# Performance work log

Measured on AMD Instinct MI355X. Metric: run time of the kernel, lower is better.

## Reference

```python
import jax, jax.numpy as jnp
import numpy as np

B, S, E = 4, 2048, 512
H, D = 8, 64
MIN_W, MAX_W = 256, 1024
EPS = 1e-6


def setup_inputs() -> dict:
    key = jax.random.key(0)
    ks = jax.random.split(key, 9)
    w = lambda k, shp: jax.random.normal(k, shp, dtype=jnp.float32) * 0.02
    return {
        "x": jax.random.normal(ks[0], (B, S, E), dtype=jnp.float32),
        "rms1_w": jnp.ones((E,), jnp.float32),
        "rms2_w": jnp.ones((E,), jnp.float32),
        "qkv_w": w(ks[1], (3 * E, E)),
        "out_w": w(ks[2], (E, E)),
        "cs_w1": w(ks[3], (E // 4, E)),
        "cs_w2": w(ks[4], (1, E // 4)),
        "gate_w": w(ks[5], (2304, E)),
        "up_w": w(ks[6], (2304, E)),
        "down_w": w(ks[7], (E, 2304)),
    }


def _rmsnorm(x, w):
    rms = jax.lax.rsqrt(jnp.mean(x * x, axis=-1, keepdims=True) + EPS)
    return x * rms * w


def _rotate_half(x):
    x1 = x[..., ::2]
    x2 = x[..., 1::2]
    return jnp.stack((-x2, x1), axis=-1).reshape(x.shape)


def reference(x, rms1_w, rms2_w, qkv_w, out_w, cs_w1, cs_w2, gate_w, up_w, down_w):
    # --- pre-norm ---
    h = _rmsnorm(x, rms1_w)                                  # [B,S,E]
    # --- qkv ---
    qkv = h @ qkv_w.T                                        # [B,S,3E]
    qkv = qkv.reshape(B, S, 3, H, D).transpose(2, 0, 3, 1, 4)
    q, k, v = qkv[0], qkv[1], qkv[2]                         # [B,H,S,D]
    # --- RoPE (cat-freqs cos/sin + interleaved rotate_half, as in source) ---
    inv_freq = 1.0 / (10000.0 ** (jnp.arange(0, D, 2, dtype=jnp.float32) / D))
    pos = jnp.arange(S, dtype=jnp.float32)
    freqs = jnp.outer(pos, inv_freq)                         # [S,D/2]
    emb = jnp.concatenate([freqs, freqs], axis=-1)           # [S,D]
    cos = jnp.cos(emb)[None, None]
    sin = jnp.sin(emb)[None, None]
    q = q * cos + _rotate_half(q) * sin
    k = k * cos + _rotate_half(k) * sin
    # --- attention scores ---
    scale = D ** -0.5
    scores = jnp.einsum("bhqd,bhkd->bhqk", q, k) * scale     # [B,H,S,S]
    # --- complexity -> dynamic window size ---
    n = S * E
    mu = jnp.mean(h, axis=(1, 2), keepdims=True)
    var = jnp.sum((h - mu) ** 2, axis=(1, 2)) / (n - 1)      # unbiased, per batch
    var_norm = jax.nn.sigmoid(var * 10.0 - 5.0)
    xm = jnp.mean(h, axis=1)                                 # [B,E]
    learned = jax.nn.sigmoid((jax.nn.silu(xm @ cs_w1.T)) @ cs_w2.T)[:, 0]
    complexity = (var_norm + learned) / 2.0                  # [B]
    ws_f = MIN_W + jnp.mean(complexity) * (MAX_W - MIN_W)
    ws = ws_f.astype(jnp.int32)                              # trunc, like .int()
    ws = jnp.maximum(jnp.minimum(ws, S), MIN_W)
    # --- causal + sliding-window mask ---
    p = jnp.arange(S)
    rel = p[:, None] - p[None, :]                            # [S,S]
    allowed = (rel >= 0) & (rel < ws)
    scores = jnp.where(allowed[None, None], scores, -jnp.inf)
    attn = jax.nn.softmax(scores, axis=-1)
    out = jnp.einsum("bhqk,bhkd->bhqd", attn, v)             # [B,H,S,D]
    out = out.transpose(0, 2, 1, 3).reshape(B, S, E)
    out = out @ out_w.T
    x = x + out
    # --- SwiGLU FFN ---
    h2 = _rmsnorm(x, rms2_w)
    ffn = (jax.nn.silu(h2 @ gate_w.T) * (h2 @ up_w.T)) @ down_w.T
    return x + ffn
```

## Files before the change

kernel.cpp:

```cpp
#include <hip/hip_runtime.h>

typedef unsigned short u16;
typedef unsigned int   u32;
typedef __attribute__((ext_vector_type(4))) float  f32x4;
typedef __attribute__((ext_vector_type(8))) __bf16 bf16x8;
typedef __attribute__((ext_vector_type(4))) u32    u32x4;
typedef __attribute__((ext_vector_type(2))) u32    u32x2;

#define B_ 4
#define S_ 2048
#define E_ 512
#define H_ 8
#define D_ 64

__device__ __forceinline__ u16 f2bf(float f) {
  union { float f; u32 u; } a; a.f = f;
  u32 r = a.u + 0x7FFFu + ((a.u >> 16) & 1u);
  return (u16)(r >> 16);
}
__device__ __forceinline__ float bf2f(u16 u) {
  union { u32 u; float f; } a; a.u = (u32)u << 16;
  return a.f;
}
__device__ __forceinline__ u32 pkbf(float lo, float hi) {
  u32 r;
  asm("v_cvt_pk_bf16_f32 %0, %1, %2" : "=v"(r) : "v"(lo), "v"(hi));
  return r;
}

#define GLOAD16(gp, lp) __builtin_amdgcn_global_load_lds( \
    (const __attribute__((address_space(1))) void*)(gp),  \
    (__attribute__((address_space(3))) void*)(lp), 16, 0, 0)

__global__ __launch_bounds__(256) void cvt_k(const float* __restrict__ s,
                                             u16* __restrict__ d, int n) {
  int i = (blockIdx.x * 256 + threadIdx.x) * 4;
  if (i >= n) return;
  f32x4 v = *(const f32x4*)(s + i);
  u32x2 o;
  o.x = pkbf(v[0], v[1]);
  o.y = pkbf(v[2], v[3]);
  *(u32x2*)(d + i) = o;
}

__global__ __launch_bounds__(256) void ropetab_k(float* __restrict__ ct,
                                                 float* __restrict__ st) {
  int idx = blockIdx.x * 256 + threadIdx.x;
  int s = idx >> 6, j = idx & 63;
  float f = powf(10000.f, -(float)(j & 31) * (1.f / 32.f));
  float ang = (float)s * f;
  ct[idx] = cosf(ang);
  st[idx] = sinf(ang);
}

__global__ __launch_bounds__(256) void rmsnorm_k(const float* __restrict__ x,
                                                 const float* __restrict__ wv,
                                                 u16* __restrict__ o) {
  const int row = blockIdx.x;
  const int t = threadIdx.x;
  const float* xr = x + (size_t)row * E_;
  float v0 = xr[t], v1 = xr[t + 256];
  float ss = v0 * v0 + v1 * v1;
#pragma unroll
  for (int m = 1; m < 64; m <<= 1) ss += __shfl_xor(ss, m, 64);
  __shared__ float red[4];
  if ((t & 63) == 0) red[t >> 6] = ss;
  __syncthreads();
  float tot = red[0] + red[1] + red[2] + red[3];
  float rms = 1.f / sqrtf(tot * (1.f / (float)E_) + 1e-6f);
  o[(size_t)row * E_ + t]       = f2bf(v0 * rms * wv[t]);
  o[(size_t)row * E_ + t + 256] = f2bf(v1 * rms * wv[t + 256]);
}

__global__ __launch_bounds__(256) void colsum_k(const u16* __restrict__ h,
                                                float* __restrict__ st) {
  const int b = blockIdx.x >> 3, ck = blockIdx.x & 7;
  const u16* hb = h + ((size_t)b * S_ + ck * 256) * E_;
  const int t = threadIdx.x;
  float a0 = 0, a1 = 0, s = 0, sq = 0;
  for (int r = 0; r < 256; ++r) {
    float v0 = bf2f(hb[(size_t)r * E_ + t]);
    float v1 = bf2f(hb[(size_t)r * E_ + t + 256]);
    a0 += v0; a1 += v1;
    s += v0 + v1; sq += v0 * v0 + v1 * v1;
  }
  atomicAdd(&st[8 + b * E_ + t], a0);
  atomicAdd(&st[8 + b * E_ + t + 256], a1);
#pragma unroll
  for (int m = 1; m < 64; m <<= 1) { s += __shfl_xor(s, m, 64); sq += __shfl_xor(sq, m, 64); }
  if ((t & 63) == 0) { atomicAdd(&st[b], s); atomicAdd(&st[4 + b], sq); }
}

__global__ __launch_bounds__(128) void wscalc_k(float* __restrict__ st,
                                                const float* __restrict__ w1,
                                                const float* __restrict__ w2) {
  const int j = threadIdx.x;
  __shared__ float comp[4];
  __shared__ float tw[2];
  float dot[4] = {0.f, 0.f, 0.f, 0.f};
  const float* w1r = w1 + (size_t)j * E_;
  for (int e = 0; e < E_; ++e) {
    float wv = w1r[e];
    dot[0] += st[8 + 0 * E_ + e] * wv;
    dot[1] += st[8 + 1 * E_ + e] * wv;
    dot[2] += st[8 + 2 * E_ + e] * wv;
    dot[3] += st[8 + 3 * E_ + e] * wv;
  }
  for (int b = 0; b < 4; ++b) {
    float d = dot[b] * (1.f / (float)S_);
    float si = d / (1.f + __expf(-d));
    float term = si * w2[j];
#pragma unroll
    for (int m = 1; m < 64; m <<= 1) term += __shfl_xor(term, m, 64);
    __syncthreads();
    if ((j & 63) == 0) tw[j >> 6] = term;
    __syncthreads();
    if (j == 0) {
      float pre = tw[0] + tw[1];
      float learned = 1.f / (1.f + __expf(-pre));
      const float n = (float)S_ * (float)E_;
      float sum = st[b], ssq = st[4 + b];
      float var = (ssq - sum * sum / n) / (n - 1.f);
      float vn = 1.f / (1.f + __expf(-(var * 10.f - 5.f)));
      comp[b] = 0.5f * (vn + learned);
    }
    __syncthreads();
  }
  if (j == 0) {
    float mean = 0.25f * (comp[0] + comp[1] + comp[2] + comp[3]);
    float wsf = 256.f + mean * 768.f;
    int v = (int)wsf;
    v = v < 256 ? 256 : (v > S_ ? S_ : v);
    ((int*)st)[2056] = v;
  }
}

struct EpiArgs {
  u16* q; u16* k; u16* vt;
  const float* cosT; const float* sinT;
  const float* resid; float* outf;
};

template <int N, int K, int EPI, int WAVES>
__global__ __launch_bounds__(WAVES * 64) void gemm_k(const u16* __restrict__ A,
                                                     const u16* __restrict__ W,
                                                     EpiArgs ea) {
  constexpr int NBN = N / 128;
  __shared__ u16 sA[2][128 * 32];
  __shared__ u16 sB[2][128 * 32];
  const int tid = threadIdx.x;
  const int nwg = (int)gridDim.x;
  const int bid = (int)blockIdx.x;
  const int logical = (bid & 7) * (nwg >> 3) + (bid >> 3);
  const int bm = logical / NBN, bn = logical % NBN;
  const int lane = tid & 63, w = tid >> 6;
  const int g = lane >> 4, c = lane & 15;
  constexpr int MI = (WAVES == 4) ? 4 : 2;
  const int wrow = (w >> 1) * ((WAVES == 4) ? 64 : 32);
  const int wcol = (w & 1) * 64;

  const int srow = tid >> 2, sch = tid & 3;
  const u16* gA = A + (size_t)(bm * 128 + srow) * K + sch * 8;
  const u16* gB = W + (size_t)(bn * 128 + srow) * K + sch * 8;
  const int lofs = w * 1024;

  f32x4 acc[MI][4];
  f32x4 zz = {0.f, 0.f, 0.f, 0.f};
#pragma unroll
  for (int i = 0; i < MI; ++i)
#pragma unroll
    for (int j = 0; j < 4; ++j) acc[i][j] = zz;

  auto stage = [&](int buf, int ko) {
    GLOAD16(gA + ko, (char*)sA[buf] + lofs);
    GLOAD16(gB + ko, (char*)sB[buf] + lofs);
    if constexpr (WAVES == 4) {
      GLOAD16(gA + (size_t)64 * K + ko, (char*)sA[buf] + lofs + 4096);
      GLOAD16(gB + (size_t)64 * K + ko, (char*)sB[buf] + lofs + 4096);
    }
  };

  constexpr int NIT = K / 32;
  stage(0, 0);
  __syncthreads();
  int cur = 0;
  for (int it = 0; it < NIT; ++it) {
    if (it + 1 < NIT) stage(cur ^ 1, (it + 1) * 32);
    const u16* bufA = sA[cur];
    const u16* bufB = sB[cur];
    bf16x8 af[MI], bfr[4];
#pragma unroll
    for (int mi = 0; mi < MI; ++mi)
      af[mi] = *(const bf16x8*)&bufA[(wrow + mi * 16 + c) * 32 + g * 8];
#pragma unroll
    for (int nj = 0; nj < 4; ++nj)
      bfr[nj] = *(const bf16x8*)&bufB[(wcol + nj * 16 + c) * 32 + g * 8];
#pragma unroll
    for (int mi = 0; mi < MI; ++mi)
#pragma unroll
      for (int nj = 0; nj < 4; ++nj)
        acc[mi][nj] = __builtin_amdgcn_mfma_f32_16x16x32_bf16(af[mi], bfr[nj], acc[mi][nj], 0, 0, 0);
    __syncthreads();
    cur ^= 1;
  }

#pragma unroll
  for (int mi = 0; mi < MI; ++mi) {
#pragma unroll
    for (int nj = 0; nj < 4; ++nj) {
      const int rowb = bm * 128 + wrow + mi * 16 + 4 * g;
      const int cc = bn * 128 + wcol + nj * 16 + c;
      if constexpr (EPI == 0) {
        const int which = cc >> 9;
        const int hh = (cc >> 6) & 7;
        const int d = cc & 63;
        const int bi = rowb >> 11;
        const int s = rowb & (S_ - 1);
        if (which == 2) {
          u32x2 pk;
          pk.x = pkbf(acc[mi][nj][0], acc[mi][nj][1]);
          pk.y = pkbf(acc[mi][nj][2], acc[mi][nj][3]);
          *(u32x2*)(ea.vt + (((size_t)(bi * H_ + hh) * D_ + d) * S_ + s)) = pk;
        } else {
          u16* dst = (which == 0 ? ea.q : ea.k) + (((size_t)(bi * H_ + hh) * S_ + s) * D_ + d);
#pragma unroll
          for (int r = 0; r < 4; ++r) {
            float v = acc[mi][nj][r];
            float pv = __shfl_xor(v, 1, 64);
            int si = s + r;
            float cs = ea.cosT[si * 64 + d];
            float sn = ea.sinT[si * 64 + d];
            float o = v * cs + ((d & 1) ? pv : -pv) * sn;
            dst[(size_t)r * D_] = f2bf(o);
          }
        }
      } else {
#pragma unroll
        for (int r = 0; r < 4; ++r) {
          size_t idx = (size_t)(rowb + r) * N + cc;
          ea.outf[idx] = acc[mi][nj][r] + ea.resid[idx];
        }
      }
    }
  }
}

__global__ __launch_bounds__(512) void gemmgu_k(const u16* __restrict__ A,
                                                const u16* __restrict__ Wg,
                                                const u16* __restrict__ Wu,
                                                u16* __restrict__ outb) {
  __shared__ u16 sA[2][128 * 32];
  __shared__ u16 sG[2][128 * 32];
  __shared__ u16 sU[2][128 * 32];
  const int tid = threadIdx.x;
  const int nwg = (int)gridDim.x;
  const int bid = (int)blockIdx.x;
  const int logical = (bid & 7) * (nwg >> 3) + (bid >> 3);
  const int bm = logical / 18, bn = logical % 18;
  const int lane = tid & 63, w = tid >> 6;
  const int g = lane >> 4, c = lane & 15;
  const int wrow = (w >> 1) * 32;
  const int wcol = (w & 1) * 64;

  const int srow = tid >> 2, sch = tid & 3;
  const u16* gA = A + (size_t)(bm * 128 + srow) * 512 + sch * 8;
  const u16* gG = Wg + (size_t)(bn * 128 + srow) * 512 + sch * 8;
  const u16* gU = Wu + (size_t)(bn * 128 + srow) * 512 + sch * 8;
  const int lofs = w * 1024;

  f32x4 accg[2][4], accu[2][4];
  f32x4 zz = {0.f, 0.f, 0.f, 0.f};
#pragma unroll
  for (int i = 0; i < 2; ++i)
#pragma unroll
    for (int j = 0; j < 4; ++j) { accg[i][j] = zz; accu[i][j] = zz; }

  auto stage = [&](int buf, int ko) {
    GLOAD16(gA + ko, (char*)sA[buf] + lofs);
    GLOAD16(gG + ko, (char*)sG[buf] + lofs);
    GLOAD16(gU + ko, (char*)sU[buf] + lofs);
  };

  stage(0, 0);
  __syncthreads();
  int cur = 0;
  for (int it = 0; it < 16; ++it) {
    if (it + 1 < 16) stage(cur ^ 1, (it + 1) * 32);
    const u16* bufA = sA[cur];
    const u16* bufG = sG[cur];
    const u16* bufU = sU[cur];
    bf16x8 af[2], bg[4], bu[4];
#pragma unroll
    for (int mi = 0; mi < 2; ++mi)
      af[mi] = *(const bf16x8*)&bufA[(wrow + mi * 16 + c) * 32 + g * 8];
#pragma unroll
    for (int nj = 0; nj < 4; ++nj) {
      bg[nj] = *(const bf16x8*)&bufG[(wcol + nj * 16 + c) * 32 + g * 8];
      bu[nj] = *(const bf16x8*)&bufU[(wcol + nj * 16 + c) * 32 + g * 8];
    }
#pragma unroll
    for (int mi = 0; mi < 2; ++mi)
#pragma unroll
      for (int nj = 0; nj < 4; ++nj) {
        accg[mi][nj] = __builtin_amdgcn_mfma_f32_16x16x32_bf16(af[mi], bg[nj], accg[mi][nj], 0, 0, 0);
        accu[mi][nj] = __builtin_amdgcn_mfma_f32_16x16x32_bf16(af[mi], bu[nj], accu[mi][nj], 0, 0, 0);
      }
    __syncthreads();
    cur ^= 1;
  }

#pragma unroll
  for (int mi = 0; mi < 2; ++mi) {
#pragma unroll
    for (int nj = 0; nj < 4; ++nj) {
      const int rowb = bm * 128 + wrow + mi * 16 + 4 * g;
      const int cc = bn * 128 + wcol + nj * 16 + c;
#pragma unroll
      for (int r = 0; r < 4; ++r) {
        float gv = accg[mi][nj][r];
        float uv = accu[mi][nj][r];
        float sil = gv / (1.f + __expf(-gv));
        outb[(size_t)(rowb + r) * 2304 + cc] = f2bf(sil * uv);
      }
    }
  }
}

__global__ __launch_bounds__(256) void attn_k(const u16* __restrict__ Qb,
                                              const u16* __restrict__ Kb,
                                              const u16* __restrict__ Vt,
                                              u16* __restrict__ ao,
                                              const int* __restrict__ wsp) {
  const int bh = blockIdx.x;
  const int b = bh >> 3, h = bh & 7;
  const int qt = blockIdx.y;
  const int tid = threadIdx.x;
  const int w = tid >> 6, lane = tid & 63;
  const int g = lane >> 4, c = lane & 15;
  const int ws = *wsp;
  const int qw = qt * 64 + w * 16;
  const u16* Qh = Qb + (size_t)bh * S_ * D_;
  const u16* Kh = Kb + (size_t)bh * S_ * D_;
  const u16* Vh = Vt + (size_t)bh * D_ * S_;

  bf16x8 qf0 = *(const bf16x8*)(Qh + (qw + c) * D_ + g * 8);
  bf16x8 qf1 = *(const bf16x8*)(Qh + (qw + c) * D_ + 32 + g * 8);

  const float SCL = 0.125f * 1.44269504089f;
  float m2 = -3e38f, lsum = 0.f;
  f32x4 O[4];
  f32x4 zz = {0.f, 0.f, 0.f, 0.f};
#pragma unroll
  for (int i = 0; i < 4; ++i) O[i] = zz;

  int lo = qw - ws + 1;
  if (lo < 0) lo = 0;
  const int q = qw + c;
  for (int kb = lo & ~63; kb <= qw + 15; kb += 64) {
    bf16x8 kf[4][2];
#pragma unroll
    for (int t = 0; t < 4; ++t) {
      const u16* kp = Kh + (kb + 16 * t + c) * D_;
      kf[t][0] = *(const bf16x8*)(kp + g * 8);
      kf[t][1] = *(const bf16x8*)(kp + 32 + g * 8);
    }
    f32x4 st4[4];
    __builtin_amdgcn_s_setprio(1);
#pragma unroll
    for (int t = 0; t < 4; ++t) {
      f32x4 s = zz;
      s = __builtin_amdgcn_mfma_f32_16x16x32_bf16(kf[t][0], qf0, s, 0, 0, 0);
      s = __builtin_amdgcn_mfma_f32_16x16x32_bf16(kf[t][1], qf1, s, 0, 0, 0);
      st4[t] = s;
    }
    __builtin_amdgcn_s_setprio(0);
    bf16x8 vf[4][2];
#pragma unroll
    for (int dt = 0; dt < 4; ++dt) {
      const u16* vp = Vh + (size_t)(dt * 16 + c) * S_ + kb;
      vf[dt][0] = *(const bf16x8*)(vp + g * 8);
      vf[dt][1] = *(const bf16x8*)(vp + 32 + g * 8);
    }
    const bool interior = (kb + 63 <= qw) && (kb >= qw + 16 - ws);
    float p[4][4];
    float bm = -3e38f;
    if (interior) {
#pragma unroll
      for (int t = 0; t < 4; ++t)
#pragma unroll
        for (int r = 0; r < 4; ++r) {
          p[t][r] = st4[t][r] * SCL;
          bm = fmaxf(bm, p[t][r]);
        }
    } else {
#pragma unroll
      for (int t = 0; t < 4; ++t)
#pragma unroll
        for (int r = 0; r < 4; ++r) {
          int ki = kb + 16 * t + 4 * g + r;
          float v = st4[t][r] * SCL;
          bool ok = (q >= ki) && (q - ki) < ws;
          p[t][r] = ok ? v : -__builtin_inff();
          bm = fmaxf(bm, p[t][r]);
        }
    }
    bm = fmaxf(bm, __shfl_xor(bm, 16, 64));
    bm = fmaxf(bm, __shfl_xor(bm, 32, 64));
    if (!__all(bm - m2 <= 8.f)) {
      float mnew = fmaxf(m2, bm);
      float al = exp2f(m2 - mnew);
      lsum *= al;
#pragma unroll
      for (int i = 0; i < 4; ++i) O[i] *= al;
      m2 = mnew;
    }
    float psum = 0.f;
#pragma unroll
    for (int t = 0; t < 4; ++t)
#pragma unroll
      for (int r = 0; r < 4; ++r) {
        p[t][r] = exp2f(p[t][r] - m2);
        psum += p[t][r];
      }
    psum += __shfl_xor(psum, 16, 64);
    psum += __shfl_xor(psum, 32, 64);
    lsum += psum;

    u32 pp[4][2];
#pragma unroll
    for (int t = 0; t < 4; ++t) {
      pp[t][0] = pkbf(p[t][0], p[t][1]);
      pp[t][1] = pkbf(p[t][2], p[t][3]);
    }
    const int lA = (g & 1) * 32 + c;
    const int lB = lA + 16;
    const int hi = g >> 1;
    union { bf16x8 v; u32 u[4]; } pf0, pf1;
#pragma unroll
    for (int wi = 0; wi < 2; ++wi) {
      u32 a0 = (u32)__shfl((int)pp[0][wi], lA, 64);
      u32 a1 = (u32)__shfl((int)pp[1][wi], lA, 64);
      u32 a2 = (u32)__shfl((int)pp[2][wi], lA, 64);
      u32 a3 = (u32)__shfl((int)pp[3][wi], lA, 64);
      u32 b0 = (u32)__shfl((int)pp[0][wi], lB, 64);
      u32 b1 = (u32)__shfl((int)pp[1][wi], lB, 64);
      u32 b2 = (u32)__shfl((int)pp[2][wi], lB, 64);
      u32 b3 = (u32)__shfl((int)pp[3][wi], lB, 64);
      pf0.u[wi]     = hi ? a1 : a0;
      pf0.u[2 + wi] = hi ? b1 : b0;
      pf1.u[wi]     = hi ? a3 : a2;
      pf1.u[2 + wi] = hi ? b3 : b2;
    }
    __builtin_amdgcn_s_setprio(1);
#pragma unroll
    for (int dt = 0; dt < 4; ++dt) {
      O[dt] = __builtin_amdgcn_mfma_f32_16x16x32_bf16(vf[dt][0], pf0.v, O[dt], 0, 0, 0);
      O[dt] = __builtin_amdgcn_mfma_f32_16x16x32_bf16(vf[dt][1], pf1.v, O[dt], 0, 0, 0);
    }
    __builtin_amdgcn_s_setprio(0);
  }

  float inv = 1.f / lsum;
  __shared__ u16 ob[4][16][80];
#pragma unroll
  for (int dt = 0; dt < 4; ++dt)
#pragma unroll
    for (int r = 0; r < 4; ++r)
      ob[w][c][dt * 16 + 4 * g + r] = f2bf(O[dt][r] * inv);
  __syncthreads();
#pragma unroll
  for (int it = 0; it < 2; ++it) {
    int linear = tid + it * 256;
    int qrow = linear >> 3, ch = linear & 7;
    u32x4 v = *(const u32x4*)&ob[qrow >> 4][qrow & 15][ch * 8];
    *(u32x4*)(ao + ((size_t)(b * S_ + qt * 64 + qrow)) * E_ + h * D_ + ch * 8) = v;
  }
}

extern "C" void kernel_launch(void* const* d_in, const int* in_sizes, int n_in,
                              void* d_out, int out_size, void* d_ws, size_t ws_size,
                              hipStream_t stream) {
  const float* x      = (const float*)d_in[0];
  const float* rms1_w = (const float*)d_in[1];
  const float* rms2_w = (const float*)d_in[2];
  const float* qkv_w  = (const float*)d_in[3];
  const float* out_w  = (const float*)d_in[4];
  const float* cs_w1  = (const float*)d_in[5];
  const float* cs_w2  = (const float*)d_in[6];
  const float* gate_w = (const float*)d_in[7];
  const float* up_w   = (const float*)d_in[8];
  const float* down_w = (const float*)d_in[9];

  char* ws = (char*)d_ws;
  constexpr size_t o_wqkv = 0;
  constexpr size_t o_wout = 1572864;
  constexpr size_t o_wgate = 2097152;
  constexpr size_t o_wup = 4456448;
  constexpr size_t o_wdown = 6815744;
  constexpr size_t o_h = 9175040;
  constexpr size_t o_stats = 17563648;
  constexpr size_t o_cos = 17580032;
  constexpr size_t o_sin = 18104320;
  constexpr size_t o_Q = 18628608;
  constexpr size_t o_K = 27017216;
  constexpr size_t o_Vt = 35405824;
  constexpr size_t o_x2 = 43794432;
  constexpr size_t o_gate = 60571648;

  u16* wqkv = (u16*)(ws + o_wqkv);
  u16* wout = (u16*)(ws + o_wout);
  u16* wgate = (u16*)(ws + o_wgate);
  u16* wup = (u16*)(ws + o_wup);
  u16* wdown = (u16*)(ws + o_wdown);
  u16* h = (u16*)(ws + o_h);
  float* stats = (float*)(ws + o_stats);
  float* cosT = (float*)(ws + o_cos);
  float* sinT = (float*)(ws + o_sin);
  u16* Qb = (u16*)(ws + o_Q);
  u16* Kb = (u16*)(ws + o_K);
  u16* Vt = (u16*)(ws + o_Vt);
  float* x2 = (float*)(ws + o_x2);
  u16* gateb = (u16*)(ws + o_gate);
  u16* attno = h;
  u16* h2 = Qb;

  hipMemsetAsync(stats, 0, 16384, stream);
  cvt_k<<<768, 256, 0, stream>>>(qkv_w, wqkv, 1536 * 512);
  cvt_k<<<256, 256, 0, stream>>>(out_w, wout, 512 * 512);
  cvt_k<<<1152, 256, 0, stream>>>(gate_w, wgate, 2304 * 512);
  cvt_k<<<1152, 256, 0, stream>>>(up_w, wup, 2304 * 512);
  cvt_k<<<1152, 256, 0, stream>>>(down_w, wdown, 512 * 2304);
  ropetab_k<<<512, 256, 0, stream>>>(cosT, sinT);

  rmsnorm_k<<<8192, 256, 0, stream>>>(x, rms1_w, h);
  colsum_k<<<32, 256, 0, stream>>>(h, stats);
  wscalc_k<<<1, 128, 0, stream>>>(stats, cs_w1, cs_w2);

  EpiArgs ea{};
  ea.q = Qb; ea.k = Kb; ea.vt = Vt; ea.cosT = cosT; ea.sinT = sinT;
  gemm_k<1536, 512, 0, 4><<<768, 256, 0, stream>>>(h, wqkv, ea);

  attn_k<<<dim3(32, 32), 256, 0, stream>>>(Qb, Kb, Vt, attno, (const int*)(stats + 2056));

  EpiArgs e2{};
  e2.resid = x; e2.outf = x2;
  gemm_k<512, 512, 1, 8><<<256, 512, 0, stream>>>(attno, wout, e2);

  rmsnorm_k<<<8192, 256, 0, stream>>>(x2, rms2_w, h2);

  gemmgu_k<<<1152, 512, 0, stream>>>(h2, wgate, wup, gateb);

  EpiArgs e5{};
  e5.resid = x2; e5.outf = (float*)d_out;
  gemm_k<512, 2304, 1, 8><<<256, 512, 0, stream>>>(gateb, wdown, e5);

  (void)in_sizes; (void)n_in; (void)out_size; (void)ws_size;
}
```

Baseline: 407.8 us.

## Swizzle GEMM LDS layout, fine-grained vmcnt waits, smaller reversed attention blocks

GEMM kernels now XOR-swizzle the 16-byte chunk index when staging tiles into LDS so the fragment reads avoid bank conflicts. The post-stage __syncthreads is replaced with explicit vmcnt waits and raw s_barrier, so the prefetch of the next tile keeps running during compute. Attention blocks shrink from 4 waves over 64 queries to 2 waves over 32 queries on a 1D grid, with the heaviest (latest) query tiles scheduled first for better load balance. The raw barriers and manual waitcnt rely on exact load counts per stage, which makes the code fragile if staging changes.

```diff
diff --git a/kernel.cpp b/kernel.cpp
--- a/kernel.cpp
+++ b/kernel.cpp
@@ -31,6 +31,8 @@
 #define GLOAD16(gp, lp) __builtin_amdgcn_global_load_lds( \
     (const __attribute__((address_space(1))) void*)(gp),  \
     (__attribute__((address_space(3))) void*)(lp), 16, 0, 0)
+
+#define BARRIER() asm volatile("s_barrier" ::: "memory")
 
 __global__ __launch_bounds__(256) void cvt_k(const float* __restrict__ s,
                                              u16* __restrict__ d, int n) {
@@ -159,9 +161,10 @@
   const int wrow = (w >> 1) * ((WAVES == 4) ? 64 : 32);
   const int wcol = (w & 1) * 64;
 
-  const int srow = tid >> 2, sch = tid & 3;
-  const u16* gA = A + (size_t)(bm * 128 + srow) * K + sch * 8;
-  const u16* gB = W + (size_t)(bn * 128 + srow) * K + sch * 8;
+  const int sr0 = w * 16 + (lane >> 2);
+  const int ch0 = (lane & 3) ^ ((sr0 >> 1) & 3);
+  const u16* gA = A + (size_t)(bm * 128 + sr0) * K + ch0 * 8;
+  const u16* gB = W + (size_t)(bn * 128 + sr0) * K + ch0 * 8;
   const int lofs = w * 1024;
 
   f32x4 acc[MI][4];
@@ -182,25 +185,35 @@
 
   constexpr int NIT = K / 32;
   stage(0, 0);
-  __syncthreads();
   int cur = 0;
   for (int it = 0; it < NIT; ++it) {
-    if (it + 1 < NIT) stage(cur ^ 1, (it + 1) * 32);
+    if (it + 1 < NIT) {
+      stage(cur ^ 1, (it + 1) * 32);
+      if constexpr (WAVES == 4) asm volatile("s_waitcnt vmcnt(4)" ::: "memory");
+      else                      asm volatile("s_waitcnt vmcnt(2)" ::: "memory");
+    } else {
+      asm volatile("s_waitcnt vmcnt(0)" ::: "memory");
+    }
+    BARRIER();
     const u16* bufA = sA[cur];
     const u16* bufB = sB[cur];
     bf16x8 af[MI], bfr[4];
 #pragma unroll
-    for (int mi = 0; mi < MI; ++mi)
-      af[mi] = *(const bf16x8*)&bufA[(wrow + mi * 16 + c) * 32 + g * 8];
-#pragma unroll
-    for (int nj = 0; nj < 4; ++nj)
-      bfr[nj] = *(const bf16x8*)&bufB[(wcol + nj * 16 + c) * 32 + g * 8];
+    for (int mi = 0; mi < MI; ++mi) {
+      int ar = wrow + mi * 16 + c;
+      af[mi] = *(const bf16x8*)&bufA[ar * 32 + ((g ^ ((ar >> 1) & 3)) * 8)];
+    }
+#pragma unroll
+    for (int nj = 0; nj < 4; ++nj) {
+      int br = wcol + nj * 16 + c;
+      bfr[nj] = *(const bf16x8*)&bufB[br * 32 + ((g ^ ((br >> 1) & 3)) * 8)];
+    }
 #pragma unroll
     for (int mi = 0; mi < MI; ++mi)
 #pragma unroll
       for (int nj = 0; nj < 4; ++nj)
         acc[mi][nj] = __builtin_amdgcn_mfma_f32_16x16x32_bf16(af[mi], bfr[nj], acc[mi][nj], 0, 0, 0);
-    __syncthreads();
+    BARRIER();
     cur ^= 1;
   }
 
@@ -262,10 +275,11 @@
   const int wrow = (w >> 1) * 32;
   const int wcol = (w & 1) * 64;
 
-  const int srow = tid >> 2, sch = tid & 3;
-  const u16* gA = A + (size_t)(bm * 128 + srow) * 512 + sch * 8;
-  const u16* gG = Wg + (size_t)(bn * 128 + srow) * 512 + sch * 8;
-  const u16* gU = Wu + (size_t)(bn * 128 + srow) * 512 + sch * 8;
+  const int sr0 = w * 16 + (lane >> 2);
+  const int ch0 = (lane & 3) ^ ((sr0 >> 1) & 3);
+  const u16* gA = A + (size_t)(bm * 128 + sr0) * 512 + ch0 * 8;
+  const u16* gG = Wg + (size_t)(bn * 128 + sr0) * 512 + ch0 * 8;
+  const u16* gU = Wu + (size_t)(bn * 128 + sr0) * 512 + ch0 * 8;
   const int lofs = w * 1024;
 
   f32x4 accg[2][4], accu[2][4];
@@ -282,21 +296,30 @@
   };
 
   stage(0, 0);
-  __syncthreads();
   int cur = 0;
   for (int it = 0; it < 16; ++it) {
-    if (it + 1 < 16) stage(cur ^ 1, (it + 1) * 32);
+    if (it + 1 < 16) {
+      stage(cur ^ 1, (it + 1) * 32);
+      asm volatile("s_waitcnt vmcnt(3)" ::: "memory");
+    } else {
+      asm volatile("s_waitcnt vmcnt(0)" ::: "memory");
+    }
+    BARRIER();
     const u16* bufA = sA[cur];
     const u16* bufG = sG[cur];
     const u16* bufU = sU[cur];
     bf16x8 af[2], bg[4], bu[4];
 #pragma unroll
-    for (int mi = 0; mi < 2; ++mi)
-      af[mi] = *(const bf16x8*)&bufA[(wrow + mi * 16 + c) * 32 + g * 8];
+    for (int mi = 0; mi < 2; ++mi) {
+      int ar = wrow + mi * 16 + c;
+      af[mi] = *(const bf16x8*)&bufA[ar * 32 + ((g ^ ((ar >> 1) & 3)) * 8)];
+    }
 #pragma unroll
     for (int nj = 0; nj < 4; ++nj) {
-      bg[nj] = *(const bf16x8*)&bufG[(wcol + nj * 16 + c) * 32 + g * 8];
-      bu[nj] = *(const bf16x8*)&bufU[(wcol + nj * 16 + c) * 32 + g * 8];
+      int br = wcol + nj * 16 + c;
+      int sw = (g ^ ((br >> 1) & 3)) * 8;
+      bg[nj] = *(const bf16x8*)&bufG[br * 32 + sw];
+      bu[nj] = *(const bf16x8*)&bufU[br * 32 + sw];
     }
 #pragma unroll
     for (int mi = 0; mi < 2; ++mi)
@@ -305,7 +328,7 @@
         accg[mi][nj] = __builtin_amdgcn_mfma_f32_16x16x32_bf16(af[mi], bg[nj], accg[mi][nj], 0, 0, 0);
         accu[mi][nj] = __builtin_amdgcn_mfma_f32_16x16x32_bf16(af[mi], bu[nj], accu[mi][nj], 0, 0, 0);
       }
-    __syncthreads();
+    BARRIER();
     cur ^= 1;
   }
 
@@ -326,19 +349,20 @@
   }
 }
 
-__global__ __launch_bounds__(256) void attn_k(const u16* __restrict__ Qb,
+__global__ __launch_bounds__(128) void attn_k(const u16* __restrict__ Qb,
                                               const u16* __restrict__ Kb,
                                               const u16* __restrict__ Vt,
                                               u16* __restrict__ ao,
                                               const int* __restrict__ wsp) {
-  const int bh = blockIdx.x;
+  const int bid = (int)blockIdx.x;
+  const int qh = 63 - (bid >> 5);
+  const int bh = bid & 31;
   const int b = bh >> 3, h = bh & 7;
-  const int qt = blockIdx.y;
   const int tid = threadIdx.x;
   const int w = tid >> 6, lane = tid & 63;
   const int g = lane >> 4, c = lane & 15;
   const int ws = *wsp;
-  const int qw = qt * 64 + w * 16;
+  const int qw = qh * 32 + w * 16;
   const u16* Qh = Qb + (size_t)bh * S_ * D_;
   const u16* Kh = Kb + (size_t)bh * S_ * D_;
   const u16* Vh = Vt + (size_t)bh * D_ * S_;
@@ -461,7 +485,7 @@
   }
 
   float inv = 1.f / lsum;
-  __shared__ u16 ob[4][16][80];
+  __shared__ u16 ob[2][16][80];
 #pragma unroll
   for (int dt = 0; dt < 4; ++dt)
 #pragma unroll
@@ -470,10 +494,10 @@
   __syncthreads();
 #pragma unroll
   for (int it = 0; it < 2; ++it) {
-    int linear = tid + it * 256;
+    int linear = tid + it * 128;
     int qrow = linear >> 3, ch = linear & 7;
     u32x4 v = *(const u32x4*)&ob[qrow >> 4][qrow & 15][ch * 8];
-    *(u32x4*)(ao + ((size_t)(b * S_ + qt * 64 + qrow)) * E_ + h * D_ + ch * 8) = v;
+    *(u32x4*)(ao + ((size_t)(b * S_ + qh * 32 + qrow)) * E_ + h * D_ + ch * 8) = v;
   }
 }
 
@@ -540,7 +564,7 @@
   ea.q = Qb; ea.k = Kb; ea.vt = Vt; ea.cosT = cosT; ea.sinT = sinT;
   gemm_k<1536, 512, 0, 4><<<768, 256, 0, stream>>>(h, wqkv, ea);
 
-  attn_k<<<dim3(32, 32), 256, 0, stream>>>(Qb, Kb, Vt, attno, (const int*)(stats + 2056));
+  attn_k<<<2048, 128, 0, stream>>>(Qb, Kb, Vt, attno, (const int*)(stats + 2056));
 
   EpiArgs e2{};
   e2.resid = x; e2.outf = x2;
```

New measurement: 397.0 us. 1.03x faster.
